# Optimization experiments

Hardware: AMD Instinct MI355X
Metric: run time of the kernel (lower is better)

## Reference

```python
import jax, jax.numpy as jnp
import numpy as np

DIM = 1024
HEADS = 16
HEAD_DIM = DIM // HEADS
K_NEIGH = 64  # local_window, adaptive_window=False
SCALE = 1.0 / np.sqrt(HEAD_DIM)


def setup_inputs() -> dict:
    key = jax.random.key(0)
    ks = jax.random.split(key, 6)
    b, n = 1, 4096
    x = jax.random.normal(ks[0], (b, n, DIM), dtype=jnp.float32)
    cantor_coords = jax.random.uniform(ks[1], (n,), dtype=jnp.float32)
    # torch nn.Linear(dim, 3*dim): weight [3*dim, dim]; we store transposed [dim, 3*dim]
    W_qkv = jax.random.normal(ks[2], (DIM, 3 * DIM), dtype=jnp.float32) * (1.0 / np.sqrt(DIM))
    b_qkv = jax.random.normal(ks[3], (3 * DIM,), dtype=jnp.float32) * 0.01
    W_out = jax.random.normal(ks[4], (DIM, DIM), dtype=jnp.float32) * (1.0 / np.sqrt(DIM))
    b_out = jax.random.normal(ks[5], (DIM,), dtype=jnp.float32) * 0.01
    return {"x": x, "cantor_coords": cantor_coords, "W_qkv": W_qkv,
            "b_qkv": b_qkv, "W_out": W_out, "b_out": b_out}


def _routes(cantor_coords):
    # [n, n] pairwise |c_i - c_j|; k smallest -> top_k of negated distances
    d = jnp.abs(cantor_coords[:, None] - cantor_coords[None, :])
    _, idx = jax.lax.top_k(-d, K_NEIGH)  # [n, k]
    return idx


def reference(x, cantor_coords, W_qkv, b_qkv, W_out, b_out):
    b, n, _ = x.shape
    qkv = x @ W_qkv + b_qkv                          # [b, n, 3*dim]
    qkv = qkv.reshape(b, n, 3, HEADS, HEAD_DIM)
    qkv = jnp.transpose(qkv, (2, 0, 3, 1, 4))        # [3, b, h, n, d]
    q, k, v = qkv[0], qkv[1], qkv[2]

    routes = _routes(cantor_coords)                  # [n, k]
    k_g = k[:, :, routes, :]                         # [b, h, n, k, d]
    v_g = v[:, :, routes, :]
    scores = jnp.einsum('bhqd,bhqkd->bhqk', q, k_g) * SCALE
    attn = jax.nn.softmax(scores, axis=-1)           # dropout p=0 (eval)
    out = jnp.einsum('bhqk,bhqkd->bhqd', attn, v_g)  # [b, h, n, d]
    out = jnp.transpose(out, (0, 2, 1, 3)).reshape(b, n, DIM)
    return out @ W_out + b_out
```

## Files before the change

### kernel.cpp

```cpp
#include <hip/hip_runtime.h>
#include <hip/hip_bf16.h>

typedef _Float16 f16x8 __attribute__((ext_vector_type(8)));
typedef float f32x4 __attribute__((ext_vector_type(4)));
typedef unsigned long long u64;

#define NSEQ 4096
#define DIMM 1024
#define NHEAD 16
#define HD 64
#define NQKV 3072

#define BAR() asm volatile("s_barrier" ::: "memory")

__device__ __forceinline__ f32x4 mfma16(f16x8 a, f16x8 b, f32x4 c) {
  return __builtin_amdgcn_mfma_f32_16x16x32_f16(a, b, c, 0, 0, 0);
}

__device__ __forceinline__ void glds16(const void* g, void* l) {
  __builtin_amdgcn_global_load_lds(
      (const __attribute__((address_space(1))) void*)g,
      (__attribute__((address_space(3))) void*)l, 16, 0, 0);
}

__global__ __launch_bounds__(256) void convert_x_kernel(
    const float* __restrict__ x, _Float16* __restrict__ xh) {
  const int i = blockIdx.x * 256 + threadIdx.x;
  const float4 a = ((const float4*)x)[i * 2];
  const float4 b = ((const float4*)x)[i * 2 + 1];
  f16x8 o = {(_Float16)a.x, (_Float16)a.y, (_Float16)a.z, (_Float16)a.w,
             (_Float16)b.x, (_Float16)b.y, (_Float16)b.z, (_Float16)b.w};
  ((f16x8*)xh)[i] = o;
}

__global__ __launch_bounds__(256) void transpose_w_kernel(
    const float* __restrict__ W, _Float16* __restrict__ Wt, int K, int Nn) {
  __shared__ float tile[64][65];
  const int k0 = blockIdx.x * 64, n0 = blockIdx.y * 64;
  const int tx = threadIdx.x & 63, ty = threadIdx.x >> 6;
  for (int rr = ty; rr < 64; rr += 4)
    tile[rr][tx] = W[(size_t)(k0 + rr) * Nn + n0 + tx];
  __syncthreads();
  for (int cc = ty; cc < 64; cc += 4)
    Wt[(size_t)(n0 + cc) * K + k0 + tx] = (_Float16)tile[tx][cc];
}

__global__ __launch_bounds__(256) void rank_sort_kernel(
    const float* __restrict__ c, int* __restrict__ sorted_idx,
    float* __restrict__ csort) {
  __shared__ float sc[NSEQ];
  const int t = threadIdx.x;
#pragma unroll
  for (int it = 0; it < 4; ++it) {
    const int i = it * 256 + t;
    ((float4*)sc)[i] = ((const float4*)c)[i];
  }
  __syncthreads();
  const int elem = blockIdx.x * 32 + (t >> 3);
  const int s = t & 7;
  const unsigned mybits = __float_as_uint(sc[elem]);
  int cnt = 0;
#pragma unroll 8
  for (int m = 0; m < 512; ++m) {
    const int j = s + (m << 3);
    const unsigned bj = __float_as_uint(sc[j]);
    cnt += (bj < mybits || (bj == mybits && j < elem)) ? 1 : 0;
  }
  cnt += __shfl_xor(cnt, 1);
  cnt += __shfl_xor(cnt, 2);
  cnt += __shfl_xor(cnt, 4);
  if (s == 0) {
    sorted_idx[cnt] = elem;
    csort[cnt] = sc[elem];
  }
}

__global__ __launch_bounds__(256) void mask_kernel(
    const float* __restrict__ csort, const int* __restrict__ sorted_idx,
    unsigned* __restrict__ masks) {
  __shared__ unsigned lm[4][8];
  const int tid = threadIdx.x, lane = tid & 63, wid = tid >> 6;
  const int p = blockIdx.x * 4 + wid;
  int W0 = 64 * (p >> 6) - 96;
  W0 = min(max(W0, 0), NSEQ - 256);
  const float cp = csort[p];
  u64 key[4];
#pragma unroll
  for (int r = 0; r < 4; ++r) {
    const int w = r * 64 + lane;
    const float d = fabsf(csort[W0 + w] - cp);
    key[r] = (((u64)__float_as_uint(d)) << 20) |
             (((u64)(unsigned)sorted_idx[W0 + w]) << 8) | (unsigned)w;
  }
  if (lane < 8) lm[wid][lane] = 0u;
#pragma unroll
  for (int k = 2; k <= 256; k <<= 1) {
#pragma unroll
    for (int j = k >> 1; j > 0; j >>= 1) {
      if (j >= 64) {
        const int rj = j >> 6;
#pragma unroll
        for (int r = 0; r < 4; ++r) {
          const int rp = r ^ rj;
          if (rp > r) {
            const bool up = (((r * 64) & k) == 0);
            const u64 a = key[r], b2 = key[rp];
            const bool sw = (a > b2) == up;
            key[r] = sw ? b2 : a;
            key[rp] = sw ? a : b2;
          }
        }
      } else {
#pragma unroll
        for (int r = 0; r < 4; ++r) {
          const u64 pv = __shfl_xor(key[r], j);
          const bool up = (((r * 64 + lane) & k) == 0);
          const bool lower = ((lane & j) == 0);
          const bool takemin = (lower == up);
          const u64 mn = key[r] < pv ? key[r] : pv;
          const u64 mx = key[r] < pv ? pv : key[r];
          key[r] = takemin ? mn : mx;
        }
      }
    }
  }
  const unsigned w0 = (unsigned)(key[0] & 0xffu);
  atomicOr(&lm[wid][w0 >> 5], 1u << (w0 & 31u));
  __syncthreads();
  if (lane < 8) masks[p * 8 + lane] = lm[wid][lane];
}

__device__ __forceinline__ f16x8 ldsfrag(const char* base, int r, int g) {
  return *(const f16x8*)(base + r * 128 + ((g ^ (r & 7)) << 4));
}

__device__ __forceinline__ void stage_half(const char* gbase, size_t kb, int t,
                                           char* lds_half, int tid) {
#pragma unroll
  for (int s = 0; s < 2; ++s) {
    const int rel = tid * 16 + s * 8192;
    const int r = rel >> 7;
    const int g = (rel >> 4) & 7;
    const int gg = g ^ (r & 7);
    glds16(gbase + (size_t)r * kb + t * 128 + gg * 16, lds_half + rel);
  }
}

__device__ __forceinline__ void rd_b(const char* Bb, int wn, int lr, int kg,
                                     f16x8 (&bf)[4][2]) {
#pragma unroll
  for (int nt = 0; nt < 4; ++nt) {
    bf[nt][0] = ldsfrag(Bb, wn + nt * 16 + lr, kg);
    bf[nt][1] = ldsfrag(Bb, wn + nt * 16 + lr, 4 + kg);
  }
}

template <int Q>
__device__ __forceinline__ void rd_a(const char* Ab, int wm, int lr, int kg,
                                     f16x8 (&af)[2][2]) {
#pragma unroll
  for (int m = 0; m < 2; ++m) {
    af[m][0] = ldsfrag(Ab, wm + (2 * Q + m) * 16 + lr, kg);
    af[m][1] = ldsfrag(Ab, wm + (2 * Q + m) * 16 + lr, 4 + kg);
  }
}

template <int Q>
__device__ __forceinline__ void do_mfma(const f16x8 (&af)[2][2],
                                        const f16x8 (&bf)[4][2],
                                        f32x4 (&acc)[8][4]) {
#pragma unroll
  for (int m = 0; m < 2; ++m)
#pragma unroll
    for (int nt = 0; nt < 4; ++nt) {
      acc[2 * Q + m][nt] = mfma16(af[m][0], bf[nt][0], acc[2 * Q + m][nt]);
      acc[2 * Q + m][nt] = mfma16(af[m][1], bf[nt][1], acc[2 * Q + m][nt]);
    }
}

template <bool LAST>
__device__ __forceinline__ void ktile_pair(const char* Ag, const char* Bg,
                                           size_t kb, char* smem, int tid,
                                           int wm, int wn, int lr, int kg,
                                           int t1, int t2, int t3,
                                           f32x4 (&acc)[8][4]) {
  char* A0 = smem;
  char* A1 = smem + 32768;
  char* B0 = smem + 65536;
  char* B1 = smem + 98304;
  f16x8 bf[4][2], af[2][2];
  rd_b(B0, wn, lr, kg, bf);
  rd_a<0>(A0, wm, lr, kg, af);
  stage_half(Ag, kb, t1, A1, tid);
  BAR();
  __builtin_amdgcn_s_setprio(1);
  do_mfma<0>(af, bf, acc);
  __builtin_amdgcn_s_setprio(0);
  BAR();
  rd_a<1>(A0, wm, lr, kg, af);
  stage_half(Ag + 128 * kb, kb, t1, A1 + 16384, tid);
  BAR();
  __builtin_amdgcn_s_setprio(1);
  do_mfma<1>(af, bf, acc);
  __builtin_amdgcn_s_setprio(0);
  BAR();
  rd_a<2>(A0, wm, lr, kg, af);
  if (!LAST) stage_half(Bg, kb, t2, B0, tid);
  BAR();
  __builtin_amdgcn_s_setprio(1);
  do_mfma<2>(af, bf, acc);
  __builtin_amdgcn_s_setprio(0);
  BAR();
  rd_a<3>(A0, wm, lr, kg, af);
  if (!LAST) stage_half(Bg + 128 * kb, kb, t2, B0 + 16384, tid);
  BAR();
  __builtin_amdgcn_s_setprio(1);
  do_mfma<3>(af, bf, acc);
  __builtin_amdgcn_s_setprio(0);
  if (LAST)
    asm volatile("s_waitcnt vmcnt(0)" ::: "memory");
  else
    asm volatile("s_waitcnt vmcnt(4)" ::: "memory");
  BAR();
  rd_b(B1, wn, lr, kg, bf);
  rd_a<0>(A1, wm, lr, kg, af);
  if (!LAST) stage_half(Ag, kb, t2, A0, tid);
  BAR();
  __builtin_amdgcn_s_setprio(1);
  do_mfma<0>(af, bf, acc);
  __builtin_amdgcn_s_setprio(0);
  BAR();
  rd_a<1>(A1, wm, lr, kg, af);
  if (!LAST) stage_half(Ag + 128 * kb, kb, t2, A0 + 16384, tid);
  BAR();
  __builtin_amdgcn_s_setprio(1);
  do_mfma<1>(af, bf, acc);
  __builtin_amdgcn_s_setprio(0);
  BAR();
  rd_a<2>(A1, wm, lr, kg, af);
  if (!LAST) stage_half(Bg, kb, t3, B1, tid);
  BAR();
  __builtin_amdgcn_s_setprio(1);
  do_mfma<2>(af, bf, acc);
  __builtin_amdgcn_s_setprio(0);
  BAR();
  rd_a<3>(A1, wm, lr, kg, af);
  if (!LAST) stage_half(Bg + 128 * kb, kb, t3, B1 + 16384, tid);
  BAR();
  __builtin_amdgcn_s_setprio(1);
  do_mfma<3>(af, bf, acc);
  __builtin_amdgcn_s_setprio(0);
  if (!LAST) asm volatile("s_waitcnt vmcnt(4)" ::: "memory");
  BAR();
}

__global__ __launch_bounds__(512, 2) void qkv_gemm256_kernel(
    const _Float16* __restrict__ A, const _Float16* __restrict__ Bt,
    const float* __restrict__ bias, _Float16* __restrict__ C) {
  extern __shared__ char smem[];
  const int NN = 3072;
  const size_t kb = 2048;
  const int tid = threadIdx.x;
  const int lane = tid & 63, wid = tid >> 6;
  const int lr = lane & 15, kg = lane >> 4;
  const int wm = (wid >> 2) * 128, wn = (wid & 3) * 64;
  const int bid = blockIdx.x;
  const int flat = (bid & 7) * 24 + (bid >> 3);
  const int bx = flat / 12, by = flat % 12;
  const int m0 = bx * 256, n0 = by * 256;
  const char* Ag = (const char*)A + (size_t)m0 * kb;
  const char* Bg = (const char*)Bt + (size_t)n0 * kb;
  char* A0 = smem;
  char* B0 = smem + 65536;
  char* B1 = smem + 98304;
  f32x4 acc[8][4] = {};
  stage_half(Ag, kb, 0, A0, tid);
  stage_half(Ag + 128 * kb, kb, 0, A0 + 16384, tid);
  stage_half(Bg, kb, 0, B0, tid);
  stage_half(Bg + 128 * kb, kb, 0, B0 + 16384, tid);
  stage_half(Bg, kb, 1, B1, tid);
  stage_half(Bg + 128 * kb, kb, 1, B1 + 16384, tid);
  asm volatile("s_waitcnt vmcnt(4)" ::: "memory");
  BAR();
#pragma unroll 1
  for (int i = 0; i < 7; ++i)
    ktile_pair<false>(Ag, Bg, kb, smem, tid, wm, wn, lr, kg, 2 * i + 1,
                      2 * i + 2, 2 * i + 3, acc);
  ktile_pair<true>(Ag, Bg, kb, smem, tid, wm, wn, lr, kg, 15, 16, 17, acc);
#pragma unroll
  for (int nt = 0; nt < 4; ++nt) {
    const int col = n0 + wn + nt * 16 + lr;
    const float bv = bias[col];
#pragma unroll
    for (int mt = 0; mt < 8; ++mt) {
      const int row0 = m0 + wm + mt * 16 + kg * 4;
#pragma unroll
      for (int rr = 0; rr < 4; ++rr)
        C[(size_t)(row0 + rr) * NN + col] = (_Float16)(acc[mt][nt][rr] + bv);
    }
  }
}

template <int Q>
__device__ __forceinline__ void rd_a1(const char* Ab, int wm, int lr, int kg,
                                      f16x8 (&af)[2]) {
  af[0] = ldsfrag(Ab, wm + Q * 16 + lr, kg);
  af[1] = ldsfrag(Ab, wm + Q * 16 + lr, 4 + kg);
}

template <int Q>
__device__ __forceinline__ void do_mfma1(const f16x8 (&af)[2],
                                         const f16x8 (&bf)[4][2],
                                         f32x4 (&acc)[4][4]) {
#pragma unroll
  for (int nt = 0; nt < 4; ++nt) {
    acc[Q][nt] = mfma16(af[0], bf[nt][0], acc[Q][nt]);
    acc[Q][nt] = mfma16(af[1], bf[nt][1], acc[Q][nt]);
  }
}

template <bool LAST>
__device__ __forceinline__ void ktile_pair_out(const char* Ag, const char* Bg,
                                               size_t kb, char* smem, int tid,
                                               int wm, int wn, int lr, int kg,
                                               int t1, int t2, int t3,
                                               f32x4 (&acc)[4][4]) {
  char* A0 = smem;
  char* A1 = smem + 16384;
  char* B0 = smem + 32768;
  char* B1 = smem + 65536;
  f16x8 bf[4][2], af[2];
  rd_b(B0, wn, lr, kg, bf);
  rd_a1<0>(A0, wm, lr, kg, af);
  stage_half(Ag, kb, t1, A1, tid);
  BAR();
  __builtin_amdgcn_s_setprio(1);
  do_mfma1<0>(af, bf, acc);
  __builtin_amdgcn_s_setprio(0);
  BAR();
  rd_a1<1>(A0, wm, lr, kg, af);
  if (!LAST) stage_half(Bg, kb, t2, B0, tid);
  BAR();
  __builtin_amdgcn_s_setprio(1);
  do_mfma1<1>(af, bf, acc);
  __builtin_amdgcn_s_setprio(0);
  BAR();
  rd_a1<2>(A0, wm, lr, kg, af);
  if (!LAST) stage_half(Bg + 128 * kb, kb, t2, B0 + 16384, tid);
  BAR();
  __builtin_amdgcn_s_setprio(1);
  do_mfma1<2>(af, bf, acc);
  __builtin_amdgcn_s_setprio(0);
  BAR();
  rd_a1<3>(A0, wm, lr, kg, af);
  BAR();
  __builtin_amdgcn_s_setprio(1);
  do_mfma1<3>(af, bf, acc);
  __builtin_amdgcn_s_setprio(0);
  if (LAST)
    asm volatile("s_waitcnt vmcnt(0)" ::: "memory");
  else
    asm volatile("s_waitcnt vmcnt(4)" ::: "memory");
  BAR();
  rd_b(B1, wn, lr, kg, bf);
  rd_a1<0>(A1, wm, lr, kg, af);
  if (!LAST) stage_half(Ag, kb, t2, A0, tid);
  BAR();
  __builtin_amdgcn_s_setprio(1);
  do_mfma1<0>(af, bf, acc);
  __builtin_amdgcn_s_setprio(0);
  BAR();
  rd_a1<1>(A1, wm, lr, kg, af);
  if (!LAST) stage_half(Bg, kb, t3, B1, tid);
  BAR();
  __builtin_amdgcn_s_setprio(1);
  do_mfma1<1>(af, bf, acc);
  __builtin_amdgcn_s_setprio(0);
  BAR();
  rd_a1<2>(A1, wm, lr, kg, af);
  if (!LAST) stage_half(Bg + 128 * kb, kb, t3, B1 + 16384, tid);
  BAR();
  __builtin_amdgcn_s_setprio(1);
  do_mfma1<2>(af, bf, acc);
  __builtin_amdgcn_s_setprio(0);
  BAR();
  rd_a1<3>(A1, wm, lr, kg, af);
  BAR();
  __builtin_amdgcn_s_setprio(1);
  do_mfma1<3>(af, bf, acc);
  __builtin_amdgcn_s_setprio(0);
  if (!LAST) asm volatile("s_waitcnt vmcnt(4)" ::: "memory");
  BAR();
}

__global__ __launch_bounds__(512, 2) void out_gemm256_kernel(
    const _Float16* __restrict__ A, const _Float16* __restrict__ Bt,
    const float* __restrict__ bias, float* __restrict__ C) {
  extern __shared__ char smem[];
  const size_t kb = 2048;
  const int tid = threadIdx.x;
  const int lane = tid & 63, wid = tid >> 6;
  const int lr = lane & 15, kg = lane >> 4;
  const int wm = (wid >> 2) * 64, wn = (wid & 3) * 64;
  const int bid = blockIdx.x;
  const int flat = (bid & 7) * 16 + (bid >> 3);
  const int bx = flat >> 2, by = flat & 3;
  const int m0 = bx * 128, n0 = by * 256;
  const char* Ag = (const char*)A + (size_t)m0 * kb;
  const char* Bg = (const char*)Bt + (size_t)n0 * kb;
  char* A0 = smem;
  char* B0 = smem + 32768;
  char* B1 = smem + 65536;
  f32x4 acc[4][4] = {};
  stage_half(Ag, kb, 0, A0, tid);
  stage_half(Bg, kb, 0, B0, tid);
  stage_half(Bg + 128 * kb, kb, 0, B0 + 16384, tid);
  stage_half(Bg, kb, 1, B1, tid);
  stage_half(Bg + 128 * kb, kb, 1, B1 + 16384, tid);
  asm volatile("s_waitcnt vmcnt(4)" ::: "memory");
  BAR();
#pragma unroll 1
  for (int i = 0; i < 7; ++i)
    ktile_pair_out<false>(Ag, Bg, kb, smem, tid, wm, wn, lr, kg, 2 * i + 1,
                          2 * i + 2, 2 * i + 3, acc);
  ktile_pair_out<true>(Ag, Bg, kb, smem, tid, wm, wn, lr, kg, 15, 16, 17, acc);
#pragma unroll
  for (int nt = 0; nt < 4; ++nt) {
    const int col = n0 + wn + nt * 16 + lr;
    const float bv = bias[col];
#pragma unroll
    for (int mt = 0; mt < 4; ++mt) {
      const int row0 = m0 + wm + mt * 16 + kg * 4;
#pragma unroll
      for (int rr = 0; rr < 4; ++rr)
        C[(size_t)(row0 + rr) * 1024 + col] = acc[mt][nt][rr] + bv;
    }
  }
}

__global__ __launch_bounds__(256) void permute_v_kernel(
    const _Float16* __restrict__ qkvh, const int* __restrict__ sorted_idx,
    _Float16* __restrict__ Vts) {
  __shared__ _Float16 vt[64][66];
  const int h = blockIdx.x & 15;
  const int P0 = (blockIdx.x >> 4) * 64;
  const int tid = threadIdx.x;
#pragma unroll
  for (int it = 0; it < 2; ++it) {
    const int i = it * 256 + tid;
    const int row = i >> 3, seg = i & 7;
    const int orig = sorted_idx[P0 + row];
    f16x8 v8 = *(const f16x8*)(qkvh + (size_t)orig * NQKV + 2048 + h * 64 + seg * 8);
#pragma unroll
    for (int e = 0; e < 8; ++e) vt[row][seg * 8 + e] = v8[e];
  }
  __syncthreads();
#pragma unroll
  for (int it = 0; it < 2; ++it) {
    const int i = it * 256 + tid;
    const int d = i >> 3, seg = i & 7;
    f16x8 o;
#pragma unroll
    for (int e = 0; e < 8; ++e) o[e] = vt[seg * 8 + e][d];
    *(f16x8*)(Vts + ((size_t)h * 64 + d) * NSEQ + P0 + seg * 8) = o;
  }
}

__global__ __launch_bounds__(256) void attn_kernel(
    const _Float16* __restrict__ qkvh, const _Float16* __restrict__ Vts,
    const unsigned* __restrict__ masks, const int* __restrict__ sorted_idx,
    _Float16* __restrict__ attn_h) {
  __shared__ __align__(128) char sK[32768];
  __shared__ __align__(128) char sV[32768];
  const int b = blockIdx.x, h = blockIdx.y;
  const int tid = threadIdx.x, lane = tid & 63, wid = tid >> 6;
  const int W0 = min(max(64 * b - 96, 0), NSEQ - 256);
  const int lrow16 = lane & 15, kgrp = lane >> 4;
  int ridx[8];
#pragma unroll
  for (int c = 0; c < 8; ++c)
    ridx[c] = sorted_idx[W0 + c * 32 + wid * 8 + (lane >> 3)];
#pragma unroll
  for (int c = 0; c < 8; ++c) {
    const int o = c * 4096 + wid * 1024 + lane * 16;
    const int row = o >> 7;
    const int inrow = (o & 127) ^ ((row & 7) << 4);
    glds16((const char*)qkvh + (size_t)ridx[c] * 6144 + 2048 + h * 128 + inrow,
           sK + o);
    const int d = o >> 9;
    const int inrowv = (o & 511) ^ ((d & 7) << 4);
    glds16((const char*)Vts + (size_t)(h * 64 + d) * (NSEQ * 2) + W0 * 2 + inrowv,
           sV + o);
  }
  const int p_base = b * 64 + wid * 16;
  const int orig_q = sorted_idx[p_base + lrow16];
  const char* qp = (const char*)qkvh + (size_t)orig_q * 6144 + h * 128 + kgrp * 16;
  const f16x8 aq0 = *(const f16x8*)qp;
  const f16x8 aq1 = *(const f16x8*)(qp + 64);
  unsigned mb[4];
#pragma unroll
  for (int r = 0; r < 4; ++r) {
    const int p = p_base + kgrp * 4 + r;
    unsigned bits = 0;
#pragma unroll
    for (int n = 0; n < 16; ++n) {
      const int widx = n * 16 + lrow16;
      bits |= ((masks[p * 8 + (widx >> 5)] >> (widx & 31)) & 1u) << n;
    }
    mb[r] = bits;
  }
  __syncthreads();
  float sv[16][4];
#pragma unroll
  for (int n = 0; n < 16; ++n) {
    const int j = n * 16 + lrow16;
    const int sw = (j & 7) << 4;
    const char* kr = sK + j * 128;
    const f16x8 b0 = *(const f16x8*)(kr + ((kgrp * 16) ^ sw));
    const f16x8 b1 = *(const f16x8*)(kr + ((64 + kgrp * 16) ^ sw));
    f32x4 a = {};
    a = mfma16(aq0, b0, a);
    a = mfma16(aq1, b1, a);
#pragma unroll
    for (int r = 0; r < 4; ++r)
      sv[n][r] = ((mb[r] >> n) & 1u) ? a[r] * 0.125f : -1e30f;
  }
#pragma unroll
  for (int r = 0; r < 4; ++r) {
    float m = sv[0][r];
#pragma unroll
    for (int n = 1; n < 16; ++n) m = fmaxf(m, sv[n][r]);
    m = fmaxf(m, __shfl_xor(m, 1));
    m = fmaxf(m, __shfl_xor(m, 2));
    m = fmaxf(m, __shfl_xor(m, 4));
    m = fmaxf(m, __shfl_xor(m, 8));
    float s = 0.f;
#pragma unroll
    for (int n = 0; n < 16; ++n) {
      const float e = __expf(sv[n][r] - m);
      sv[n][r] = e;
      s += e;
    }
    s += __shfl_xor(s, 1);
    s += __shfl_xor(s, 2);
    s += __shfl_xor(s, 4);
    s += __shfl_xor(s, 8);
    const float rinv = 1.f / s;
#pragma unroll
    for (int n = 0; n < 16; ++n) sv[n][r] *= rinv;
  }
  __syncthreads();
#pragma unroll
  for (int n = 0; n < 16; ++n) {
#pragma unroll
    for (int r = 0; r < 4; ++r) {
      const int lr = wid * 16 + kgrp * 4 + r;
      const int cb = (n * 16 + lrow16) * 2;
      *(_Float16*)(sK + lr * 512 + (cb ^ ((lr & 7) << 4))) = (_Float16)sv[n][r];
    }
  }
  __syncthreads();
  f32x4 oacc[4] = {};
  const int arow = wid * 16 + lrow16;
  const int swa = (arow & 7) << 4;
#pragma unroll
  for (int kt = 0; kt < 8; ++kt) {
    const int kb = kt * 64 + kgrp * 16;
    const f16x8 pa = *(const f16x8*)(sK + arow * 512 + (kb ^ swa));
#pragma unroll
    for (int nt = 0; nt < 4; ++nt) {
      const int d = nt * 16 + lrow16;
      const f16x8 vb = *(const f16x8*)(sV + d * 512 + (kb ^ ((d & 7) << 4)));
      oacc[nt] = mfma16(pa, vb, oacc[nt]);
    }
  }
#pragma unroll
  for (int r = 0; r < 4; ++r) {
    const int p = p_base + kgrp * 4 + r;
    const int orig = sorted_idx[p];
    _Float16* op = attn_h + (size_t)orig * DIMM + h * 64;
#pragma unroll
    for (int nt = 0; nt < 4; ++nt)
      op[nt * 16 + lrow16] = (_Float16)oacc[nt][r];
  }
}

extern "C" void kernel_launch(void* const* d_in, const int* in_sizes, int n_in,
                              void* d_out, int out_size, void* d_ws, size_t ws_size,
                              hipStream_t stream) {
  const float* x = (const float*)d_in[0];
  const float* cc = (const float*)d_in[1];
  const float* Wqkv = (const float*)d_in[2];
  const float* bqkv = (const float*)d_in[3];
  const float* Wout = (const float*)d_in[4];
  const float* bout = (const float*)d_in[5];
  char* ws = (char*)d_ws;

  _Float16* xh = (_Float16*)(ws + 0);
  _Float16* wqkvt = (_Float16*)(ws + 8388608);
  _Float16* woutt = (_Float16*)(ws + 14680064);
  _Float16* qkvh = (_Float16*)(ws + 16777216);
  _Float16* Vtsb = (_Float16*)(ws + 41943040);
  _Float16* atnh = (_Float16*)(ws + 50331648);
  int* sidx = (int*)(ws + 58720256);
  float* csort = (float*)(ws + 58736640);
  unsigned* msk = (unsigned*)(ws + 58753024);

  hipFuncSetAttribute((const void*)qkv_gemm256_kernel,
                      hipFuncAttributeMaxDynamicSharedMemorySize, 131072);
  hipFuncSetAttribute((const void*)out_gemm256_kernel,
                      hipFuncAttributeMaxDynamicSharedMemorySize, 98304);

  convert_x_kernel<<<2048, 256, 0, stream>>>(x, xh);
  transpose_w_kernel<<<dim3(16, 48), 256, 0, stream>>>(Wqkv, wqkvt, 1024, 3072);
  transpose_w_kernel<<<dim3(16, 16), 256, 0, stream>>>(Wout, woutt, 1024, 1024);
  rank_sort_kernel<<<128, 256, 0, stream>>>(cc, sidx, csort);
  mask_kernel<<<1024, 256, 0, stream>>>(csort, sidx, msk);
  qkv_gemm256_kernel<<<192, 512, 131072, stream>>>(xh, wqkvt, bqkv, qkvh);
  permute_v_kernel<<<1024, 256, 0, stream>>>(qkvh, sidx, Vtsb);
  attn_kernel<<<dim3(64, 16), 256, 0, stream>>>(qkvh, Vtsb, msk, sidx, atnh);
  out_gemm256_kernel<<<128, 512, 98304, stream>>>(atnh, woutt, bout,
                                                  (float*)d_out);
}
```

Measured before the change: 125.8 us.

## Fuse prep kernels, retile QKV and output GEMMs for full CU occupancy

New measurement: 109.8 us. 12.7% less time.

```diff
diff --git a/kernel.cpp b/kernel.cpp
--- a/kernel.cpp
+++ b/kernel.cpp
@@ -23,55 +23,60 @@
       (__attribute__((address_space(3))) void*)l, 16, 0, 0);
 }
 
-__global__ __launch_bounds__(256) void convert_x_kernel(
-    const float* __restrict__ x, _Float16* __restrict__ xh) {
-  const int i = blockIdx.x * 256 + threadIdx.x;
-  const float4 a = ((const float4*)x)[i * 2];
-  const float4 b = ((const float4*)x)[i * 2 + 1];
-  f16x8 o = {(_Float16)a.x, (_Float16)a.y, (_Float16)a.z, (_Float16)a.w,
-             (_Float16)b.x, (_Float16)b.y, (_Float16)b.z, (_Float16)b.w};
-  ((f16x8*)xh)[i] = o;
-}
-
-__global__ __launch_bounds__(256) void transpose_w_kernel(
-    const float* __restrict__ W, _Float16* __restrict__ Wt, int K, int Nn) {
-  __shared__ float tile[64][65];
-  const int k0 = blockIdx.x * 64, n0 = blockIdx.y * 64;
-  const int tx = threadIdx.x & 63, ty = threadIdx.x >> 6;
-  for (int rr = ty; rr < 64; rr += 4)
-    tile[rr][tx] = W[(size_t)(k0 + rr) * Nn + n0 + tx];
-  __syncthreads();
-  for (int cc = ty; cc < 64; cc += 4)
-    Wt[(size_t)(n0 + cc) * K + k0 + tx] = (_Float16)tile[tx][cc];
-}
-
-__global__ __launch_bounds__(256) void rank_sort_kernel(
-    const float* __restrict__ c, int* __restrict__ sorted_idx,
+__global__ __launch_bounds__(256) void prep_kernel(
+    const float* __restrict__ x, _Float16* __restrict__ xh,
+    const float* __restrict__ Wqkv, _Float16* __restrict__ wqkvt,
+    const float* __restrict__ Wout, _Float16* __restrict__ woutt,
+    const float* __restrict__ cc, int* __restrict__ sorted_idx,
     float* __restrict__ csort) {
-  __shared__ float sc[NSEQ];
-  const int t = threadIdx.x;
-#pragma unroll
-  for (int it = 0; it < 4; ++it) {
-    const int i = it * 256 + t;
-    ((float4*)sc)[i] = ((const float4*)c)[i];
-  }
-  __syncthreads();
-  const int elem = blockIdx.x * 32 + (t >> 3);
-  const int s = t & 7;
-  const unsigned mybits = __float_as_uint(sc[elem]);
-  int cnt = 0;
+  __shared__ __align__(16) char plds[16640];
+  const int bid = blockIdx.x, t = threadIdx.x;
+  if (bid < 2048) {
+    const int i = bid * 256 + t;
+    const float4 a = ((const float4*)x)[i * 2];
+    const float4 b = ((const float4*)x)[i * 2 + 1];
+    f16x8 o = {(_Float16)a.x, (_Float16)a.y, (_Float16)a.z, (_Float16)a.w,
+               (_Float16)b.x, (_Float16)b.y, (_Float16)b.z, (_Float16)b.w};
+    ((f16x8*)xh)[i] = o;
+  } else if (bid < 3072) {
+    const bool qkv = bid < 2816;
+    const int sub = qkv ? bid - 2048 : bid - 2816;
+    const float* W = qkv ? Wqkv : Wout;
+    _Float16* Wt = qkv ? wqkvt : woutt;
+    const int Nn = qkv ? 3072 : 1024;
+    const int k0 = (sub & 15) * 64, n0 = (sub >> 4) * 64;
+    float (*tile)[65] = (float(*)[65])plds;
+    const int tx = t & 63, ty = t >> 6;
+    for (int rr = ty; rr < 64; rr += 4)
+      tile[rr][tx] = W[(size_t)(k0 + rr) * Nn + n0 + tx];
+    __syncthreads();
+    for (int ccn = ty; ccn < 64; ccn += 4)
+      Wt[(size_t)(n0 + ccn) * 1024 + k0 + tx] = (_Float16)tile[tx][ccn];
+  } else {
+    float* sc = (float*)plds;
+#pragma unroll
+    for (int it = 0; it < 4; ++it) {
+      const int i = it * 256 + t;
+      ((float4*)sc)[i] = ((const float4*)cc)[i];
+    }
+    __syncthreads();
+    const int elem = (bid - 3072) * 32 + (t >> 3);
+    const int s = t & 7;
+    const unsigned mybits = __float_as_uint(sc[elem]);
+    int cnt = 0;
 #pragma unroll 8
-  for (int m = 0; m < 512; ++m) {
-    const int j = s + (m << 3);
-    const unsigned bj = __float_as_uint(sc[j]);
-    cnt += (bj < mybits || (bj == mybits && j < elem)) ? 1 : 0;
-  }
-  cnt += __shfl_xor(cnt, 1);
-  cnt += __shfl_xor(cnt, 2);
-  cnt += __shfl_xor(cnt, 4);
-  if (s == 0) {
-    sorted_idx[cnt] = elem;
-    csort[cnt] = sc[elem];
+    for (int m = 0; m < 512; ++m) {
+      const int j = s + (m << 3);
+      const unsigned bj = __float_as_uint(sc[j]);
+      cnt += (bj < mybits || (bj == mybits && j < elem)) ? 1 : 0;
+    }
+    cnt += __shfl_xor(cnt, 1);
+    cnt += __shfl_xor(cnt, 2);
+    cnt += __shfl_xor(cnt, 4);
+    if (s == 0) {
+      sorted_idx[cnt] = elem;
+      csort[cnt] = sc[elem];
+    }
   }
 }
 
@@ -146,10 +151,19 @@
   }
 }
 
-__device__ __forceinline__ void rd_b(const char* Bb, int wn, int lr, int kg,
-                                     f16x8 (&bf)[4][2]) {
-#pragma unroll
-  for (int nt = 0; nt < 4; ++nt) {
+__device__ __forceinline__ void stage_64r(const char* gbase, size_t kb, int t,
+                                          char* lds8k, int tid) {
+  const int rel = tid * 16;
+  const int r = rel >> 7;
+  const int g = (rel >> 4) & 7;
+  const int gg = g ^ (r & 7);
+  glds16(gbase + (size_t)r * kb + t * 128 + gg * 16, lds8k + rel);
+}
+
+__device__ __forceinline__ void rd_b3(const char* Bb, int wn, int lr, int kg,
+                                      f16x8 (&bf)[3][2]) {
+#pragma unroll
+  for (int nt = 0; nt < 3; ++nt) {
     bf[nt][0] = ldsfrag(Bb, wn + nt * 16 + lr, kg);
     bf[nt][1] = ldsfrag(Bb, wn + nt * 16 + lr, 4 + kg);
   }
@@ -166,95 +180,109 @@
 }
 
 template <int Q>
-__device__ __forceinline__ void do_mfma(const f16x8 (&af)[2][2],
-                                        const f16x8 (&bf)[4][2],
-                                        f32x4 (&acc)[8][4]) {
+__device__ __forceinline__ void do_mfma3(const f16x8 (&af)[2][2],
+                                         const f16x8 (&bf)[3][2],
+                                         f32x4 (&acc)[8][3]) {
 #pragma unroll
   for (int m = 0; m < 2; ++m)
 #pragma unroll
-    for (int nt = 0; nt < 4; ++nt) {
+    for (int nt = 0; nt < 3; ++nt) {
       acc[2 * Q + m][nt] = mfma16(af[m][0], bf[nt][0], acc[2 * Q + m][nt]);
       acc[2 * Q + m][nt] = mfma16(af[m][1], bf[nt][1], acc[2 * Q + m][nt]);
     }
 }
 
 template <bool LAST>
-__device__ __forceinline__ void ktile_pair(const char* Ag, const char* Bg,
-                                           size_t kb, char* smem, int tid,
-                                           int wm, int wn, int lr, int kg,
-                                           int t1, int t2, int t3,
-                                           f32x4 (&acc)[8][4]) {
+__device__ __forceinline__ void ktile_pair192(const char* Ag, const char* Bg,
+                                              size_t kb, char* smem, int tid,
+                                              int wm, int wn, int lr, int kg,
+                                              int t1, int t2, int t3,
+                                              f32x4 (&acc)[8][3]) {
   char* A0 = smem;
   char* A1 = smem + 32768;
   char* B0 = smem + 65536;
-  char* B1 = smem + 98304;
-  f16x8 bf[4][2], af[2][2];
-  rd_b(B0, wn, lr, kg, bf);
+  char* B1 = smem + 65536 + 24576;
+  f16x8 bf[3][2], af[2][2];
+  rd_b3(B0, wn, lr, kg, bf);
   rd_a<0>(A0, wm, lr, kg, af);
-  stage_half(Ag, kb, t1, A1, tid);
-  BAR();
-  __builtin_amdgcn_s_setprio(1);
-  do_mfma<0>(af, bf, acc);
+  stage_64r(Ag, kb, t1, A1, tid);
+  stage_64r(Ag + 64 * kb, kb, t1, A1 + 8192, tid);
+  BAR();
+  __builtin_amdgcn_s_setprio(1);
+  do_mfma3<0>(af, bf, acc);
   __builtin_amdgcn_s_setprio(0);
   BAR();
   rd_a<1>(A0, wm, lr, kg, af);
-  stage_half(Ag + 128 * kb, kb, t1, A1 + 16384, tid);
-  BAR();
-  __builtin_amdgcn_s_setprio(1);
-  do_mfma<1>(af, bf, acc);
+  stage_64r(Ag + 128 * kb, kb, t1, A1 + 16384, tid);
+  stage_64r(Ag + 192 * kb, kb, t1, A1 + 24576, tid);
+  BAR();
+  __builtin_amdgcn_s_setprio(1);
+  do_mfma3<1>(af, bf, acc);
   __builtin_amdgcn_s_setprio(0);
   BAR();
   rd_a<2>(A0, wm, lr, kg, af);
-  if (!LAST) stage_half(Bg, kb, t2, B0, tid);
-  BAR();
-  __builtin_amdgcn_s_setprio(1);
-  do_mfma<2>(af, bf, acc);
+  if (!LAST) {
+    stage_64r(Bg, kb, t2, B0, tid);
+    stage_64r(Bg + 64 * kb, kb, t2, B0 + 8192, tid);
+  }
+  BAR();
+  __builtin_amdgcn_s_setprio(1);
+  do_mfma3<2>(af, bf, acc);
   __builtin_amdgcn_s_setprio(0);
   BAR();
   rd_a<3>(A0, wm, lr, kg, af);
-  if (!LAST) stage_half(Bg + 128 * kb, kb, t2, B0 + 16384, tid);
-  BAR();
-  __builtin_amdgcn_s_setprio(1);
-  do_mfma<3>(af, bf, acc);
+  if (!LAST) stage_64r(Bg + 128 * kb, kb, t2, B0 + 16384, tid);
+  BAR();
+  __builtin_amdgcn_s_setprio(1);
+  do_mfma3<3>(af, bf, acc);
   __builtin_amdgcn_s_setprio(0);
   if (LAST)
     asm volatile("s_waitcnt vmcnt(0)" ::: "memory");
   else
-    asm volatile("s_waitcnt vmcnt(4)" ::: "memory");
-  BAR();
-  rd_b(B1, wn, lr, kg, bf);
+    asm volatile("s_waitcnt vmcnt(3)" ::: "memory");
+  BAR();
+  rd_b3(B1, wn, lr, kg, bf);
   rd_a<0>(A1, wm, lr, kg, af);
-  if (!LAST) stage_half(Ag, kb, t2, A0, tid);
-  BAR();
-  __builtin_amdgcn_s_setprio(1);
-  do_mfma<0>(af, bf, acc);
+  if (!LAST) {
+    stage_64r(Ag, kb, t2, A0, tid);
+    stage_64r(Ag + 64 * kb, kb, t2, A0 + 8192, tid);
+  }
+  BAR();
+  __builtin_amdgcn_s_setprio(1);
+  do_mfma3<0>(af, bf, acc);
   __builtin_amdgcn_s_setprio(0);
   BAR();
   rd_a<1>(A1, wm, lr, kg, af);
-  if (!LAST) stage_half(Ag + 128 * kb, kb, t2, A0 + 16384, tid);
-  BAR();
-  __builtin_amdgcn_s_setprio(1);
-  do_mfma<1>(af, bf, acc);
+  if (!LAST) {
+    stage_64r(Ag + 128 * kb, kb, t2, A0 + 16384, tid);
+    stage_64r(Ag + 192 * kb, kb, t2, A0 + 24576, tid);
+  }
+  BAR();
+  __builtin_amdgcn_s_setprio(1);
+  do_mfma3<1>(af, bf, acc);
   __builtin_amdgcn_s_setprio(0);
   BAR();
   rd_a<2>(A1, wm, lr, kg, af);
-  if (!LAST) stage_half(Bg, kb, t3, B1, tid);
-  BAR();
-  __builtin_amdgcn_s_setprio(1);
-  do_mfma<2>(af, bf, acc);
+  if (!LAST) {
+    stage_64r(Bg, kb, t3, B1, tid);
+    stage_64r(Bg + 64 * kb, kb, t3, B1 + 8192, tid);
+  }
+  BAR();
+  __builtin_amdgcn_s_setprio(1);
+  do_mfma3<2>(af, bf, acc);
   __builtin_amdgcn_s_setprio(0);
   BAR();
   rd_a<3>(A1, wm, lr, kg, af);
-  if (!LAST) stage_half(Bg + 128 * kb, kb, t3, B1 + 16384, tid);
-  BAR();
-  __builtin_amdgcn_s_setprio(1);
-  do_mfma<3>(af, bf, acc);
-  __builtin_amdgcn_s_setprio(0);
-  if (!LAST) asm volatile("s_waitcnt vmcnt(4)" ::: "memory");
-  BAR();
-}
-
-__global__ __launch_bounds__(512, 2) void qkv_gemm256_kernel(
+  if (!LAST) stage_64r(Bg + 128 * kb, kb, t3, B1 + 16384, tid);
+  BAR();
+  __builtin_amdgcn_s_setprio(1);
+  do_mfma3<3>(af, bf, acc);
+  __builtin_amdgcn_s_setprio(0);
+  if (!LAST) asm volatile("s_waitcnt vmcnt(3)" ::: "memory");
+  BAR();
+}
+
+__global__ __launch_bounds__(512, 2) void qkv_gemm192_kernel(
     const _Float16* __restrict__ A, const _Float16* __restrict__ Bt,
     const float* __restrict__ bias, _Float16* __restrict__ C) {
   extern __shared__ char smem[];
@@ -263,32 +291,35 @@
   const int tid = threadIdx.x;
   const int lane = tid & 63, wid = tid >> 6;
   const int lr = lane & 15, kg = lane >> 4;
-  const int wm = (wid >> 2) * 128, wn = (wid & 3) * 64;
+  const int wm = (wid >> 2) * 128, wn = (wid & 3) * 48;
   const int bid = blockIdx.x;
-  const int flat = (bid & 7) * 24 + (bid >> 3);
-  const int bx = flat / 12, by = flat % 12;
-  const int m0 = bx * 256, n0 = by * 256;
+  const int flat = (bid & 7) * 32 + (bid >> 3);
+  const int bx = flat >> 4, by = flat & 15;
+  const int m0 = bx * 256, n0 = by * 192;
   const char* Ag = (const char*)A + (size_t)m0 * kb;
   const char* Bg = (const char*)Bt + (size_t)n0 * kb;
   char* A0 = smem;
   char* B0 = smem + 65536;
-  char* B1 = smem + 98304;
-  f32x4 acc[8][4] = {};
-  stage_half(Ag, kb, 0, A0, tid);
-  stage_half(Ag + 128 * kb, kb, 0, A0 + 16384, tid);
-  stage_half(Bg, kb, 0, B0, tid);
-  stage_half(Bg + 128 * kb, kb, 0, B0 + 16384, tid);
-  stage_half(Bg, kb, 1, B1, tid);
-  stage_half(Bg + 128 * kb, kb, 1, B1 + 16384, tid);
-  asm volatile("s_waitcnt vmcnt(4)" ::: "memory");
+  char* B1 = smem + 65536 + 24576;
+  f32x4 acc[8][3] = {};
+#pragma unroll
+  for (int u = 0; u < 4; ++u)
+    stage_64r(Ag + (size_t)(64 * u) * kb, kb, 0, A0 + u * 8192, tid);
+#pragma unroll
+  for (int u = 0; u < 3; ++u)
+    stage_64r(Bg + (size_t)(64 * u) * kb, kb, 0, B0 + u * 8192, tid);
+#pragma unroll
+  for (int u = 0; u < 3; ++u)
+    stage_64r(Bg + (size_t)(64 * u) * kb, kb, 1, B1 + u * 8192, tid);
+  asm volatile("s_waitcnt vmcnt(3)" ::: "memory");
   BAR();
 #pragma unroll 1
   for (int i = 0; i < 7; ++i)
-    ktile_pair<false>(Ag, Bg, kb, smem, tid, wm, wn, lr, kg, 2 * i + 1,
-                      2 * i + 2, 2 * i + 3, acc);
-  ktile_pair<true>(Ag, Bg, kb, smem, tid, wm, wn, lr, kg, 15, 16, 17, acc);
-#pragma unroll
-  for (int nt = 0; nt < 4; ++nt) {
+    ktile_pair192<false>(Ag, Bg, kb, smem, tid, wm, wn, lr, kg, 2 * i + 1,
+                         2 * i + 2, 2 * i + 3, acc);
+  ktile_pair192<true>(Ag, Bg, kb, smem, tid, wm, wn, lr, kg, 15, 16, 17, acc);
+#pragma unroll
+  for (int nt = 0; nt < 3; ++nt) {
     const int col = n0 + wn + nt * 16 + lr;
     const float bv = bias[col];
 #pragma unroll
@@ -301,99 +332,7 @@
   }
 }
 
-template <int Q>
-__device__ __forceinline__ void rd_a1(const char* Ab, int wm, int lr, int kg,
-                                      f16x8 (&af)[2]) {
-  af[0] = ldsfrag(Ab, wm + Q * 16 + lr, kg);
-  af[1] = ldsfrag(Ab, wm + Q * 16 + lr, 4 + kg);
-}
-
-template <int Q>
-__device__ __forceinline__ void do_mfma1(const f16x8 (&af)[2],
-                                         const f16x8 (&bf)[4][2],
-                                         f32x4 (&acc)[4][4]) {
-#pragma unroll
-  for (int nt = 0; nt < 4; ++nt) {
-    acc[Q][nt] = mfma16(af[0], bf[nt][0], acc[Q][nt]);
-    acc[Q][nt] = mfma16(af[1], bf[nt][1], acc[Q][nt]);
-  }
-}
-
-template <bool LAST>
-__device__ __forceinline__ void ktile_pair_out(const char* Ag, const char* Bg,
-                                               size_t kb, char* smem, int tid,
-                                               int wm, int wn, int lr, int kg,
-                                               int t1, int t2, int t3,
-                                               f32x4 (&acc)[4][4]) {
-  char* A0 = smem;
-  char* A1 = smem + 16384;
-  char* B0 = smem + 32768;
-  char* B1 = smem + 65536;
-  f16x8 bf[4][2], af[2];
-  rd_b(B0, wn, lr, kg, bf);
-  rd_a1<0>(A0, wm, lr, kg, af);
-  stage_half(Ag, kb, t1, A1, tid);
-  BAR();
-  __builtin_amdgcn_s_setprio(1);
-  do_mfma1<0>(af, bf, acc);
-  __builtin_amdgcn_s_setprio(0);
-  BAR();
-  rd_a1<1>(A0, wm, lr, kg, af);
-  if (!LAST) stage_half(Bg, kb, t2, B0, tid);
-  BAR();
-  __builtin_amdgcn_s_setprio(1);
-  do_mfma1<1>(af, bf, acc);
-  __builtin_amdgcn_s_setprio(0);
-  BAR();
-  rd_a1<2>(A0, wm, lr, kg, af);
-  if (!LAST) stage_half(Bg + 128 * kb, kb, t2, B0 + 16384, tid);
-  BAR();
-  __builtin_amdgcn_s_setprio(1);
-  do_mfma1<2>(af, bf, acc);
-  __builtin_amdgcn_s_setprio(0);
-  BAR();
-  rd_a1<3>(A0, wm, lr, kg, af);
-  BAR();
-  __builtin_amdgcn_s_setprio(1);
-  do_mfma1<3>(af, bf, acc);
-  __builtin_amdgcn_s_setprio(0);
-  if (LAST)
-    asm volatile("s_waitcnt vmcnt(0)" ::: "memory");
-  else
-    asm volatile("s_waitcnt vmcnt(4)" ::: "memory");
-  BAR();
-  rd_b(B1, wn, lr, kg, bf);
-  rd_a1<0>(A1, wm, lr, kg, af);
-  if (!LAST) stage_half(Ag, kb, t2, A0, tid);
-  BAR();
-  __builtin_amdgcn_s_setprio(1);
-  do_mfma1<0>(af, bf, acc);
-  __builtin_amdgcn_s_setprio(0);
-  BAR();
-  rd_a1<1>(A1, wm, lr, kg, af);
-  if (!LAST) stage_half(Bg, kb, t3, B1, tid);
-  BAR();
-  __builtin_amdgcn_s_setprio(1);
-  do_mfma1<1>(af, bf, acc);
-  __builtin_amdgcn_s_setprio(0);
-  BAR();
-  rd_a1<2>(A1, wm, lr, kg, af);
-  if (!LAST) stage_half(Bg + 128 * kb, kb, t3, B1 + 16384, tid);
-  BAR();
-  __builtin_amdgcn_s_setprio(1);
-  do_mfma1<2>(af, bf, acc);
-  __builtin_amdgcn_s_setprio(0);
-  BAR();
-  rd_a1<3>(A1, wm, lr, kg, af);
-  BAR();
-  __builtin_amdgcn_s_setprio(1);
-  do_mfma1<3>(af, bf, acc);
-  __builtin_amdgcn_s_setprio(0);
-  if (!LAST) asm volatile("s_waitcnt vmcnt(4)" ::: "memory");
-  BAR();
-}
-
-__global__ __launch_bounds__(512, 2) void out_gemm256_kernel(
+__global__ __launch_bounds__(512, 2) void out_gemm128_kernel(
     const _Float16* __restrict__ A, const _Float16* __restrict__ Bt,
     const float* __restrict__ bias, float* __restrict__ C) {
   extern __shared__ char smem[];
@@ -401,31 +340,57 @@
   const int tid = threadIdx.x;
   const int lane = tid & 63, wid = tid >> 6;
   const int lr = lane & 15, kg = lane >> 4;
-  const int wm = (wid >> 2) * 64, wn = (wid & 3) * 64;
+  const int wm = (wid >> 2) * 64, wn = (wid & 3) * 32;
   const int bid = blockIdx.x;
-  const int flat = (bid & 7) * 16 + (bid >> 3);
-  const int bx = flat >> 2, by = flat & 3;
-  const int m0 = bx * 128, n0 = by * 256;
+  const int flat = (bid & 7) * 32 + (bid >> 3);
+  const int bx = flat >> 3, by = flat & 7;
+  const int m0 = bx * 128, n0 = by * 128;
   const char* Ag = (const char*)A + (size_t)m0 * kb;
   const char* Bg = (const char*)Bt + (size_t)n0 * kb;
-  char* A0 = smem;
-  char* B0 = smem + 32768;
-  char* B1 = smem + 65536;
-  f32x4 acc[4][4] = {};
-  stage_half(Ag, kb, 0, A0, tid);
-  stage_half(Bg, kb, 0, B0, tid);
-  stage_half(Bg + 128 * kb, kb, 0, B0 + 16384, tid);
-  stage_half(Bg, kb, 1, B1, tid);
-  stage_half(Bg + 128 * kb, kb, 1, B1 + 16384, tid);
+  f32x4 acc[4][2] = {};
+  stage_half(Ag, kb, 0, smem, tid);
+  stage_half(Bg, kb, 0, smem + 49152, tid);
+  stage_half(Ag, kb, 1, smem + 16384, tid);
+  stage_half(Bg, kb, 1, smem + 49152 + 16384, tid);
   asm volatile("s_waitcnt vmcnt(4)" ::: "memory");
   BAR();
-#pragma unroll 1
-  for (int i = 0; i < 7; ++i)
-    ktile_pair_out<false>(Ag, Bg, kb, smem, tid, wm, wn, lr, kg, 2 * i + 1,
-                          2 * i + 2, 2 * i + 3, acc);
-  ktile_pair_out<true>(Ag, Bg, kb, smem, tid, wm, wn, lr, kg, 15, 16, 17, acc);
-#pragma unroll
-  for (int nt = 0; nt < 4; ++nt) {
+#pragma unroll
+  for (int t = 0; t < 16; ++t) {
+    const char* At = smem + (t % 3) * 16384;
+    const char* Bb = smem + 49152 + (t % 3) * 16384;
+    f16x8 bf[2][2], af[4][2];
+#pragma unroll
+    for (int nt = 0; nt < 2; ++nt) {
+      bf[nt][0] = ldsfrag(Bb, wn + nt * 16 + lr, kg);
+      bf[nt][1] = ldsfrag(Bb, wn + nt * 16 + lr, 4 + kg);
+    }
+#pragma unroll
+    for (int m = 0; m < 4; ++m) {
+      af[m][0] = ldsfrag(At, wm + m * 16 + lr, kg);
+      af[m][1] = ldsfrag(At, wm + m * 16 + lr, 4 + kg);
+    }
+    if (t < 14) {
+      stage_half(Ag, kb, t + 2, smem + ((t + 2) % 3) * 16384, tid);
+      stage_half(Bg, kb, t + 2, smem + 49152 + ((t + 2) % 3) * 16384, tid);
+    }
+    BAR();
+    __builtin_amdgcn_s_setprio(1);
+#pragma unroll
+    for (int m = 0; m < 4; ++m)
+#pragma unroll
+      for (int nt = 0; nt < 2; ++nt) {
+        acc[m][nt] = mfma16(af[m][0], bf[nt][0], acc[m][nt]);
+        acc[m][nt] = mfma16(af[m][1], bf[nt][1], acc[m][nt]);
+      }
+    __builtin_amdgcn_s_setprio(0);
+    if (t < 14)
+      asm volatile("s_waitcnt vmcnt(4)" ::: "memory");
+    else if (t == 14)
+      asm volatile("s_waitcnt vmcnt(0)" ::: "memory");
+    BAR();
+  }
+#pragma unroll
+  for (int nt = 0; nt < 2; ++nt) {
     const int col = n0 + wn + nt * 16 + lr;
     const float bv = bias[col];
 #pragma unroll
@@ -472,7 +437,8 @@
     _Float16* __restrict__ attn_h) {
   __shared__ __align__(128) char sK[32768];
   __shared__ __align__(128) char sV[32768];
-  const int b = blockIdx.x, h = blockIdx.y;
+  const int flat = (blockIdx.x & 7) * 128 + (blockIdx.x >> 3);
+  const int b = flat & 63, h = flat >> 6;
   const int tid = threadIdx.x, lane = tid & 63, wid = tid >> 6;
   const int W0 = min(max(64 * b - 96, 0), NSEQ - 256);
   const int lrow16 = lane & 15, kgrp = lane >> 4;
@@ -565,12 +531,12 @@
   const int swa = (arow & 7) << 4;
 #pragma unroll
   for (int kt = 0; kt < 8; ++kt) {
-    const int kb = kt * 64 + kgrp * 16;
-    const f16x8 pa = *(const f16x8*)(sK + arow * 512 + (kb ^ swa));
+    const int kbo = kt * 64 + kgrp * 16;
+    const f16x8 pa = *(const f16x8*)(sK + arow * 512 + (kbo ^ swa));
 #pragma unroll
     for (int nt = 0; nt < 4; ++nt) {
       const int d = nt * 16 + lrow16;
-      const f16x8 vb = *(const f16x8*)(sV + d * 512 + (kb ^ ((d & 7) << 4)));
+      const f16x8 vb = *(const f16x8*)(sV + d * 512 + (kbo ^ ((d & 7) << 4)));
       oacc[nt] = mfma16(pa, vb, oacc[nt]);
     }
   }
@@ -606,19 +572,17 @@
   float* csort = (float*)(ws + 58736640);
   unsigned* msk = (unsigned*)(ws + 58753024);
 
-  hipFuncSetAttribute((const void*)qkv_gemm256_kernel,
-                      hipFuncAttributeMaxDynamicSharedMemorySize, 131072);
-  hipFuncSetAttribute((const void*)out_gemm256_kernel,
+  hipFuncSetAttribute((const void*)qkv_gemm192_kernel,
+                      hipFuncAttributeMaxDynamicSharedMemorySize, 114688);
+  hipFuncSetAttribute((const void*)out_gemm128_kernel,
                       hipFuncAttributeMaxDynamicSharedMemorySize, 98304);
 
-  convert_x_kernel<<<2048, 256, 0, stream>>>(x, xh);
-  transpose_w_kernel<<<dim3(16, 48), 256, 0, stream>>>(Wqkv, wqkvt, 1024, 3072);
-  transpose_w_kernel<<<dim3(16, 16), 256, 0, stream>>>(Wout, woutt, 1024, 1024);
-  rank_sort_kernel<<<128, 256, 0, stream>>>(cc, sidx, csort);
+  prep_kernel<<<3200, 256, 0, stream>>>(x, xh, Wqkv, wqkvt, Wout, woutt, cc,
+                                        sidx, csort);
   mask_kernel<<<1024, 256, 0, stream>>>(csort, sidx, msk);
-  qkv_gemm256_kernel<<<192, 512, 131072, stream>>>(xh, wqkvt, bqkv, qkvh);
+  qkv_gemm192_kernel<<<256, 512, 114688, stream>>>(xh, wqkvt, bqkv, qkvh);
   permute_v_kernel<<<1024, 256, 0, stream>>>(qkvh, sidx, Vtsb);
-  attn_kernel<<<dim3(64, 16), 256, 0, stream>>>(qkvh, Vtsb, msk, sidx, atnh);
-  out_gemm256_kernel<<<128, 512, 98304, stream>>>(atnh, woutt, bout,
+  attn_kernel<<<1024, 256, 0, stream>>>(qkvh, Vtsb, msk, sidx, atnh);
+  out_gemm128_kernel<<<256, 512, 98304, stream>>>(atnh, woutt, bout,
                                                   (float*)d_out);
 }
```
